# Kernel tuning notes

Measured on AMD Instinct MI355X. Metric: run time of the kernel, lower is better.

## Reference

```python
import jax, jax.numpy as jnp
import numpy as np

STRIDE = 4
ANCHORS = np.array([10.0, 30.0, 60.0], dtype=np.float32)
THRESH = -3.0   # GetPBB confidence threshold
NMS_TH = 0.05   # IoU threshold from nms_idx(pbbs, 0.05)
K_CAND = 4096   # fixed candidate cap for jit-compatible greedy NMS
TOPK = 300      # __get_topk default k


def _decode(output):
    # output: [Z, H, W, A, 5] raw head output -> [N, 5] (score, z, y, x, d)
    Z, H, W, A, _ = output.shape
    dt = output.dtype
    offset = jnp.asarray((STRIDE - 1) / 2.0, dt)
    oz = (offset + STRIDE * jnp.arange(Z, dtype=dt))[:, None, None, None]
    oh = (offset + STRIDE * jnp.arange(H, dtype=dt))[None, :, None, None]
    ow = (offset + STRIDE * jnp.arange(W, dtype=dt))[None, None, :, None]
    anch = jnp.asarray(ANCHORS, dt)[None, None, None, :]
    score = output[..., 0]
    z = oz + output[..., 1] * anch
    y = oh + output[..., 2] * anch
    x = ow + output[..., 3] * anch
    d = jnp.exp(output[..., 4]) * anch
    return jnp.stack([score, z, y, x, d], axis=-1).reshape(-1, 5)


def _iou_matrix(boxes):
    # boxes: [K, 4] = (z, y, x, d) axis-aligned cubes, per iou() in source
    c = boxes[:, :3]
    r = boxes[:, 3:4] * 0.5
    s = c - r  # starts
    e = c + r  # ends
    ov = jnp.maximum(0.0, jnp.minimum(e[:, None, :], e[None, :, :])
                     - jnp.maximum(s[:, None, :], s[None, :, :]))
    inter = ov[..., 0] * ov[..., 1] * ov[..., 2]
    vol = boxes[:, 3] ** 3
    return inter / (vol[:, None] + vol[None, :] - inter)


def reference(output):
    pbb = _decode(output)  # [N, 5]
    # confidence threshold (GetPBB thresh=-3); invalid -> -inf score
    scores = jnp.where(pbb[:, 0] > THRESH, pbb[:, 0], -jnp.inf)
    top_s, idx = jax.lax.top_k(scores, K_CAND)  # sorted descending, as np.argsort(-score)
    cand = pbb[idx]                              # [K_CAND, 5]
    valid = jnp.isfinite(top_s)
    iou = jax.lax.stop_gradient(_iou_matrix(cand[:, 1:5]))  # [K, K]
    ar = jnp.arange(K_CAND)

    def body(i, keep):
        # greedy: box i (if still kept) suppresses all later boxes with IoU >= th
        sup = keep[i] & (iou[i] >= NMS_TH) & (ar > i)
        return keep & ~sup

    keep = jax.lax.fori_loop(0, K_CAND, body, valid)
    final_scores = jnp.where(keep, cand[:, 0], -jnp.inf)
    _, fidx = jax.lax.top_k(final_scores, TOPK)
    return cand[fidx]  # [TOPK, 5] top-k surviving proposals


def setup_inputs() -> dict:
    key = jax.random.key(0)
    output = jax.random.normal(key, (128, 128, 128, 3, 5), dtype=jnp.float32)
    return {"output": output}
```

## Files before the change

kernel.cpp:

```cpp
#include <hip/hip_runtime.h>
#include <stdint.h>

typedef unsigned int u32;
typedef unsigned long long u64;

#define N_BOXES 6291456
#define N_FLOAT4 7864320
#define KCAND 4096
#define TOPK 300
#define CAP 16384
#define SCORE_TH -3.0f
#define NMS_TH 0.05f
#define FIXED_TH 3.0f

#define GLD_LDS16(srcp, dstp) \
    __builtin_amdgcn_global_load_lds( \
        (const __attribute__((address_space(1))) u32*)(srcp), \
        (__attribute__((address_space(3))) u32*)(dstp), 16, 0, 0)

__device__ __forceinline__ u32 sortable(float f) {
    u32 b = __float_as_uint(f);
    return (b & 0x80000000u) ? ~b : (b | 0x80000000u);
}

__device__ __forceinline__ bool quad_score(const float4& v, u32 g, float& s, u32& bidx) {
    u32 r = (4u * g) % 5u;
    if (r == 1u) return false;
    u32 k = (r == 0u) ? 0u : (5u - r);
    s = (k == 0u) ? v.x : ((k == 1u) ? v.y : ((k == 2u) ? v.z : v.w));
    bidx = (4u * g + k) / 5u;
    return true;
}

__global__ __launch_bounds__(256) void k_scan(const float4* __restrict__ in4,
                                              u32* __restrict__ cnt,
                                              u32* __restrict__ ckey, u32* __restrict__ cidx) {
    u32 base = blockIdx.x * 256u + threadIdx.x;
    u32 hits = 0;
#pragma unroll
    for (int k = 0; k < 15; ++k) {
        u32 g = base + (u32)k * 524288u;
        float4 v = in4[g];
        float s; u32 bidx;
        if (quad_score(v, g, s, bidx) && s >= FIXED_TH) hits |= 1u << k;
    }
    while (hits) {
        int k = __builtin_ctz(hits);
        hits &= hits - 1;
        u32 g = base + (u32)k * 524288u;
        float4 v = in4[g];
        float s; u32 bidx;
        if (quad_score(v, g, s, bidx)) {
            u32 pos = atomicAdd(&cnt[0], 1u);
            if (pos < (u32)CAP) { ckey[pos] = sortable(s); cidx[pos] = bidx; }
        }
    }
}

__global__ void k_check(u32* __restrict__ cnt) {
    u32 m = cnt[0];
    u32 ok = (m >= (u32)KCAND && m <= (u32)CAP) ? 1u : 0u;
    cnt[2] = ok;
    if (!ok) cnt[0] = 0;
}

__global__ void k_hist_fb(const float* __restrict__ in, const u32* __restrict__ cnt,
                          u32* __restrict__ hist) {
    if (cnt[2] == 1u) return;
    __shared__ u32 lh[4096];
    for (int k = threadIdx.x; k < 4096; k += blockDim.x) lh[k] = 0;
    __syncthreads();
    int stride = gridDim.x * blockDim.x;
    for (int i = blockIdx.x * blockDim.x + threadIdx.x; i < N_BOXES; i += stride) {
        float f = in[(size_t)i * 5];
        u32 key = (f > SCORE_TH) ? sortable(f) : 0u;
        atomicAdd(&lh[key >> 20], 1u);
    }
    __syncthreads();
    for (int k = threadIdx.x; k < 4096; k += blockDim.x)
        if (lh[k]) atomicAdd(&hist[k], lh[k]);
}

__global__ void k_pivot_fb(const u32* __restrict__ hist, u32* __restrict__ cnt) {
    if (cnt[2] == 1u) return;
    __shared__ u32 part[256];
    int t = threadIdx.x;
    u32 s = 0;
    for (int k = 0; k < 16; ++k) s += hist[t * 16 + k];
    part[t] = s;
    __syncthreads();
    if (t == 0) {
        u32 acc = 0; int chunk = -1;
        for (int c = 255; c >= 0; --c) {
            if (acc + part[c] >= (u32)KCAND) { chunk = c; break; }
            acc += part[c];
        }
        u32 bstar = 0;
        if (chunk >= 0) {
            for (int b = chunk * 16 + 15; b >= chunk * 16; --b) {
                acc += hist[b];
                if (acc >= (u32)KCAND) { bstar = (u32)b; break; }
            }
        }
        cnt[1] = bstar;
    }
}

__global__ void k_compact_fb(const float* __restrict__ in, u32* __restrict__ cnt,
                             u32* __restrict__ ckey, u32* __restrict__ cidx) {
    if (cnt[2] == 1u) return;
    u32 bstar = cnt[1];
    int stride = gridDim.x * blockDim.x;
    for (int i = blockIdx.x * blockDim.x + threadIdx.x; i < N_BOXES; i += stride) {
        float f = in[(size_t)i * 5];
        u32 key = (f > SCORE_TH) ? sortable(f) : 0u;
        if ((key >> 20) >= bstar) {
            u32 pos = atomicAdd(&cnt[0], 1u);
            if (pos < (u32)CAP) { ckey[pos] = key; cidx[pos] = (u32)i; }
        }
    }
}

__global__ void k_rank(const u32* __restrict__ ckey, const u32* __restrict__ cidx,
                       const u32* __restrict__ cnt, u32* __restrict__ rank) {
    int M = (int)min(cnt[0], (u32)CAP);
    int e = blockIdx.x * 256 + threadIdx.x;
    bool act = (e < M);
    u32 mykey = 0, myidx = 0;
    if (act) { mykey = ckey[e]; myidx = cidx[e]; }
    int j0 = blockIdx.y * 1024;
    int j1 = min(j0 + 1024, M);
    __shared__ u32 sk[256], si[256];
    u32 r = 0;
    for (int base = j0; base < j1; base += 256) {
        __syncthreads();
        int jj = base + threadIdx.x;
        if (jj < j1) { sk[threadIdx.x] = ckey[jj]; si[threadIdx.x] = cidx[jj]; }
        __syncthreads();
        int lim = min(256, j1 - base);
        if (act) {
            for (int q = 0; q < lim; ++q) {
                u32 kq = sk[q];
                r += (u32)((kq > mykey) || (kq == mykey && si[q] < myidx));
            }
        }
    }
    if (act && r) atomicAdd(&rank[e], r);
}

__global__ void k_scatter(const u32* __restrict__ ckey, const u32* __restrict__ cidx,
                          const u32* __restrict__ cnt, const u32* __restrict__ rank,
                          u32* __restrict__ skey, u32* __restrict__ sidx) {
    int M = (int)min(cnt[0], (u32)CAP);
    int e = blockIdx.x * 256 + threadIdx.x;
    if (e < M) {
        u32 r = rank[e];
        if (r < (u32)KCAND) { skey[r] = ckey[e]; sidx[r] = cidx[e]; }
    }
}

__global__ void k_decode(const float* __restrict__ in, const u32* __restrict__ skey,
                         const u32* __restrict__ sidx, float* __restrict__ cand,
                         u64* __restrict__ keepg) {
#pragma clang fp contract(off)
    int r = blockIdx.x * 256 + threadIdx.x;
    u32 key = skey[r];
    u32 idx = sidx[r];
    u32 a = idx % 3u;
    u32 rem = idx / 3u;
    u32 w = rem & 127u; rem >>= 7;
    u32 h = rem & 127u;
    u32 z = rem >> 7;
    float anch = (a == 0u) ? 10.0f : ((a == 1u) ? 30.0f : 60.0f);
    const float* p = in + (size_t)idx * 5;
    float s  = p[0];
    float zc = (1.5f + 4.0f * (float)z) + p[1] * anch;
    float yc = (1.5f + 4.0f * (float)h) + p[2] * anch;
    float xc = (1.5f + 4.0f * (float)w) + p[3] * anch;
    float d  = expf(p[4]) * anch;
    float* o = cand + (size_t)r * 5;
    o[0] = s; o[1] = zc; o[2] = yc; o[3] = xc; o[4] = d;
    u64 bal = __ballot(key != 0u);
    if ((threadIdx.x & 63) == 0) keepg[r >> 6] = bal;
}

__global__ void k_mask(const float* __restrict__ cand, u64* __restrict__ mask) {
#pragma clang fp contract(off)
    int i = blockIdx.y;
    int wv = blockIdx.x * 4 + (threadIdx.x >> 6);
    int j = wv * 64 + (threadIdx.x & 63);
    const float* bi = cand + (size_t)i * 5;
    const float* bj = cand + (size_t)j * 5;
    float zi = bi[1], yi = bi[2], xi = bi[3], di = bi[4];
    float zj = bj[1], yj = bj[2], xj = bj[3], dj = bj[4];
    float ri = di * 0.5f, rj = dj * 0.5f;
    float ov0 = fmaxf(0.0f, fminf(zi + ri, zj + rj) - fmaxf(zi - ri, zj - rj));
    float ov1 = fmaxf(0.0f, fminf(yi + ri, yj + rj) - fmaxf(yi - ri, yj - rj));
    float ov2 = fmaxf(0.0f, fminf(xi + ri, xj + rj) - fmaxf(xi - ri, xj - rj));
    float inter = (ov0 * ov1) * ov2;
    float vi = (di * di) * di;
    float vj = (dj * dj) * dj;
    float iou = inter / ((vi + vj) - inter);
    bool bit = (j > i) && (iou >= NMS_TH);
    u64 bal = __ballot(bit);
    if ((threadIdx.x & 63) == 0) mask[(size_t)i * 64 + wv] = bal;
}

__global__ __launch_bounds__(512) void k_nms(const u64* __restrict__ mask,
                                             u64* __restrict__ keepg,
                                             u32* __restrict__ cnt) {
    __shared__ u64 tile[2][4096];
    __shared__ int sstop;
    int lane = threadIdx.x & 63;
    int wave = threadIdx.x >> 6;
    u64 K = (wave == 0) ? keepg[lane] : 0ull;
    int keptTotal = 0;
    if (threadIdx.x == 0) sstop = 64;

    {
        const char* src = (const char*)mask + wave * 4096 + lane * 16;
        char* dst = (char*)&tile[0][0] + wave * 4096;
#pragma unroll
        for (int i = 0; i < 4; ++i)
            GLD_LDS16(src + i * 1024, dst + i * 1024);
    }

    int resolved = 63;
    for (int c = 0; c < 64; ++c) {
        asm volatile("s_waitcnt vmcnt(0)" ::: "memory");
        __syncthreads();
        if (c > sstop) { resolved = sstop; break; }
        const u64* tl = &tile[c & 1][0];
        if (c + 1 < 64) {
            const char* src = (const char*)(mask + (size_t)(c + 1) * 4096) + wave * 4096 + lane * 16;
            char* dst = (char*)&tile[(c + 1) & 1][0] + wave * 4096;
#pragma unroll
            for (int i = 0; i < 4; ++i)
                GLD_LDS16(src + i * 1024, dst + i * 1024);
        }
        if (wave == 0) {
            u64 diag = tl[lane * 64 + c];
            u32 dlo = (u32)diag, dhi = (u32)(diag >> 32);
            u32 kwlo = (u32)__builtin_amdgcn_readlane((int)(u32)K, c);
            u32 kwhi = (u32)__builtin_amdgcn_readlane((int)(u32)(K >> 32), c);
            u64 remaining = ((u64)kwhi << 32) | kwlo;
            u64 kept = 0;
            while (remaining) {
                int b = __builtin_ctzll(remaining);
                kept |= 1ull << b;
                u32 rlo = (u32)__builtin_amdgcn_readlane((int)dlo, b);
                u32 rhi = (u32)__builtin_amdgcn_readlane((int)dhi, b);
                u64 rb = ((u64)rhi << 32) | rlo;
                remaining &= ~(rb | (1ull << b));
            }
            u64 s0 = 0, s1 = 0, s2 = 0, s3 = 0;
#pragma unroll
            for (int b = 0; b < 64; b += 4) {
                u64 m0 = ((kept >> (b + 0)) & 1ull) ? ~0ull : 0ull;
                u64 m1 = ((kept >> (b + 1)) & 1ull) ? ~0ull : 0ull;
                u64 m2 = ((kept >> (b + 2)) & 1ull) ? ~0ull : 0ull;
                u64 m3 = ((kept >> (b + 3)) & 1ull) ? ~0ull : 0ull;
                s0 |= tl[(b + 0) * 64 + lane] & m0;
                s1 |= tl[(b + 1) * 64 + lane] & m1;
                s2 |= tl[(b + 2) * 64 + lane] & m2;
                s3 |= tl[(b + 3) * 64 + lane] & m3;
            }
            K &= ~((s0 | s1) | (s2 | s3));
            keptTotal += (int)__popcll(kept);
            if (lane == 0 && keptTotal >= TOPK && sstop == 64) sstop = c;
        }
    }
    asm volatile("s_waitcnt vmcnt(0)" ::: "memory");
    __syncthreads();
    if (wave == 0) {
        keepg[lane] = K;
        if (lane == 0) cnt[3] = (u32)resolved;
    }
}

__global__ void k_final(const float* __restrict__ cand, const u64* __restrict__ keepg,
                        const u32* __restrict__ cnt, float* __restrict__ outp) {
    __shared__ u64 kw[64];
    __shared__ u32 wp[65];
    int t = threadIdx.x;
    int limit = (int)cnt[3];
    if (t < 64) kw[t] = (t <= limit) ? keepg[t] : 0ull;
    __syncthreads();
    if (t == 0) {
        u32 acc = 0;
        for (int wv = 0; wv < 64; ++wv) { wp[wv] = acc; acc += (u32)__popcll(kw[wv]); }
        wp[64] = acc;
    }
    __syncthreads();
    u32 nk = wp[64];
    int rmax = (limit + 1) * 64;
    for (int r = t; r < rmax; r += 256) {
        u64 word = kw[r >> 6];
        int b = r & 63;
        bool kept = (word >> b) & 1ull;
        u64 lowmask = b ? (~0ull >> (64 - b)) : 0ull;
        u32 before = wp[r >> 6] + (u32)__popcll(word & lowmask);
        u32 slot = kept ? before : (nk + (u32)r - before);
        if (slot < (u32)TOPK) {
            const float* src = cand + (size_t)r * 5;
            float* dst = outp + (size_t)slot * 5;
            dst[0] = src[0]; dst[1] = src[1]; dst[2] = src[2];
            dst[3] = src[3]; dst[4] = src[4];
        }
    }
}

extern "C" void kernel_launch(void* const* d_in, const int* in_sizes, int n_in,
                              void* d_out, int out_size, void* d_ws, size_t ws_size,
                              hipStream_t stream) {
    const float* in = (const float*)d_in[0];
    const float4* in4 = (const float4*)d_in[0];
    float* outp = (float*)d_out;
    char* ws = (char*)d_ws;

    u32* hist = (u32*)(ws + 0);
    u32* cnt  = (u32*)(ws + 16384);
    u32* rank = (u32*)(ws + 16448);
    u32* ckey = (u32*)(ws + 81984);
    u32* cidx = (u32*)(ws + 147520);
    u32* skey = (u32*)(ws + 213056);
    u32* sidx = (u32*)(ws + 229440);
    float* cand = (float*)(ws + 245824);
    u64* keepg  = (u64*)(ws + 327744);
    u64* mask   = (u64*)(ws + 328256);

    hipMemsetAsync(ws, 0, 81984, stream);

    k_scan      <<<2048, 256, 0, stream>>>(in4, cnt, ckey, cidx);
    k_check     <<<1, 1, 0, stream>>>(cnt);
    k_hist_fb   <<<1024, 256, 0, stream>>>(in, cnt, hist);
    k_pivot_fb  <<<1, 256, 0, stream>>>(hist, cnt);
    k_compact_fb<<<1024, 256, 0, stream>>>(in, cnt, ckey, cidx);
    k_rank      <<<dim3(64, 16), 256, 0, stream>>>(ckey, cidx, cnt, rank);
    k_scatter   <<<64, 256, 0, stream>>>(ckey, cidx, cnt, rank, skey, sidx);
    k_decode    <<<16, 256, 0, stream>>>(in, skey, sidx, cand, keepg);
    k_mask      <<<dim3(16, 4096), 256, 0, stream>>>(cand, mask);
    k_nms       <<<1, 512, 0, stream>>>(mask, keepg, cnt);
    k_final     <<<1, 256, 0, stream>>>(cand, keepg, cnt, outp);
}
```

Measured before the change: 175.1 us.

## Load only kept mask rows in NMS via a compact diagonal-block array

k_mask now also writes each row's diagonal 64-bit word into a compact dp array. The NMS kernel shrinks to a single wave and no longer streams the whole 32KB mask tile through LDS with double buffering each chunk. It prefetches the next diagonal block from dp and gathers only the mask rows of kept boxes straight from global memory, eight at a time. This cuts the memory traffic of the serial NMS phase and removes block barriers, but each gather now pays global-load latency where it used to read from LDS.

```diff
diff --git a/kernel.cpp b/kernel.cpp
--- a/kernel.cpp
+++ b/kernel.cpp
@@ -12,11 +12,6 @@
 #define SCORE_TH -3.0f
 #define NMS_TH 0.05f
 #define FIXED_TH 3.0f
-
-#define GLD_LDS16(srcp, dstp) \
-    __builtin_amdgcn_global_load_lds( \
-        (const __attribute__((address_space(1))) u32*)(srcp), \
-        (__attribute__((address_space(3))) u32*)(dstp), 16, 0, 0)
 
 __device__ __forceinline__ u32 sortable(float f) {
     u32 b = __float_as_uint(f);
@@ -184,7 +179,8 @@
     if ((threadIdx.x & 63) == 0) keepg[r >> 6] = bal;
 }
 
-__global__ void k_mask(const float* __restrict__ cand, u64* __restrict__ mask) {
+__global__ void k_mask(const float* __restrict__ cand, u64* __restrict__ mask,
+                       u64* __restrict__ dp) {
 #pragma clang fp contract(off)
     int i = blockIdx.y;
     int wv = blockIdx.x * 4 + (threadIdx.x >> 6);
@@ -203,79 +199,66 @@
     float iou = inter / ((vi + vj) - inter);
     bool bit = (j > i) && (iou >= NMS_TH);
     u64 bal = __ballot(bit);
-    if ((threadIdx.x & 63) == 0) mask[(size_t)i * 64 + wv] = bal;
-}
-
-__global__ __launch_bounds__(512) void k_nms(const u64* __restrict__ mask,
-                                             u64* __restrict__ keepg,
-                                             u32* __restrict__ cnt) {
-    __shared__ u64 tile[2][4096];
-    __shared__ int sstop;
-    int lane = threadIdx.x & 63;
-    int wave = threadIdx.x >> 6;
-    u64 K = (wave == 0) ? keepg[lane] : 0ull;
+    if ((threadIdx.x & 63) == 0) {
+        mask[(size_t)i * 64 + wv] = bal;
+        if (wv == (i >> 6)) dp[i] = bal;
+    }
+}
+
+__global__ __launch_bounds__(64) void k_nms(const u64* __restrict__ mask,
+                                            const u64* __restrict__ dp,
+                                            u64* __restrict__ keepg,
+                                            u32* __restrict__ cnt) {
+    int lane = threadIdx.x;
+    u64 K = keepg[lane];
     int keptTotal = 0;
-    if (threadIdx.x == 0) sstop = 64;
-
-    {
-        const char* src = (const char*)mask + wave * 4096 + lane * 16;
-        char* dst = (char*)&tile[0][0] + wave * 4096;
-#pragma unroll
-        for (int i = 0; i < 4; ++i)
-            GLD_LDS16(src + i * 1024, dst + i * 1024);
-    }
-
     int resolved = 63;
+    u64 dcur = dp[lane];
     for (int c = 0; c < 64; ++c) {
-        asm volatile("s_waitcnt vmcnt(0)" ::: "memory");
-        __syncthreads();
-        if (c > sstop) { resolved = sstop; break; }
-        const u64* tl = &tile[c & 1][0];
-        if (c + 1 < 64) {
-            const char* src = (const char*)(mask + (size_t)(c + 1) * 4096) + wave * 4096 + lane * 16;
-            char* dst = (char*)&tile[(c + 1) & 1][0] + wave * 4096;
-#pragma unroll
-            for (int i = 0; i < 4; ++i)
-                GLD_LDS16(src + i * 1024, dst + i * 1024);
-        }
-        if (wave == 0) {
-            u64 diag = tl[lane * 64 + c];
-            u32 dlo = (u32)diag, dhi = (u32)(diag >> 32);
-            u32 kwlo = (u32)__builtin_amdgcn_readlane((int)(u32)K, c);
-            u32 kwhi = (u32)__builtin_amdgcn_readlane((int)(u32)(K >> 32), c);
-            u64 remaining = ((u64)kwhi << 32) | kwlo;
-            u64 kept = 0;
-            while (remaining) {
-                int b = __builtin_ctzll(remaining);
-                kept |= 1ull << b;
-                u32 rlo = (u32)__builtin_amdgcn_readlane((int)dlo, b);
-                u32 rhi = (u32)__builtin_amdgcn_readlane((int)dhi, b);
-                u64 rb = ((u64)rhi << 32) | rlo;
-                remaining &= ~(rb | (1ull << b));
-            }
-            u64 s0 = 0, s1 = 0, s2 = 0, s3 = 0;
-#pragma unroll
-            for (int b = 0; b < 64; b += 4) {
-                u64 m0 = ((kept >> (b + 0)) & 1ull) ? ~0ull : 0ull;
-                u64 m1 = ((kept >> (b + 1)) & 1ull) ? ~0ull : 0ull;
-                u64 m2 = ((kept >> (b + 2)) & 1ull) ? ~0ull : 0ull;
-                u64 m3 = ((kept >> (b + 3)) & 1ull) ? ~0ull : 0ull;
-                s0 |= tl[(b + 0) * 64 + lane] & m0;
-                s1 |= tl[(b + 1) * 64 + lane] & m1;
-                s2 |= tl[(b + 2) * 64 + lane] & m2;
-                s3 |= tl[(b + 3) * 64 + lane] & m3;
-            }
-            K &= ~((s0 | s1) | (s2 | s3));
-            keptTotal += (int)__popcll(kept);
-            if (lane == 0 && keptTotal >= TOPK && sstop == 64) sstop = c;
-        }
-    }
-    asm volatile("s_waitcnt vmcnt(0)" ::: "memory");
-    __syncthreads();
-    if (wave == 0) {
-        keepg[lane] = K;
-        if (lane == 0) cnt[3] = (u32)resolved;
-    }
+        u64 dnext = (c + 1 < 64) ? dp[(c + 1) * 64 + lane] : 0ull;
+        u32 dlo = (u32)dcur, dhi = (u32)(dcur >> 32);
+        u32 kwlo = (u32)__builtin_amdgcn_readlane((int)(u32)K, c);
+        u32 kwhi = (u32)__builtin_amdgcn_readlane((int)(u32)(K >> 32), c);
+        u64 remaining = ((u64)kwhi << 32) | kwlo;
+        u64 kept = 0;
+        while (remaining) {
+            int b = __builtin_ctzll(remaining);
+            kept |= 1ull << b;
+            u32 rlo = (u32)__builtin_amdgcn_readlane((int)dlo, b);
+            u32 rhi = (u32)__builtin_amdgcn_readlane((int)dhi, b);
+            u64 rb = ((u64)rhi << 32) | rlo;
+            remaining &= ~(rb | (1ull << b));
+        }
+        const u64* rows = mask + (size_t)c * 4096;
+        u64 sup = 0;
+        u64 kk = kept;
+        while (kk) {
+            int b0 = __builtin_ctzll(kk); kk &= kk - 1;
+            int b1 = -1, b2 = -1, b3 = -1, b4 = -1, b5 = -1, b6 = -1, b7 = -1;
+            if (kk) { b1 = __builtin_ctzll(kk); kk &= kk - 1; }
+            if (kk) { b2 = __builtin_ctzll(kk); kk &= kk - 1; }
+            if (kk) { b3 = __builtin_ctzll(kk); kk &= kk - 1; }
+            if (kk) { b4 = __builtin_ctzll(kk); kk &= kk - 1; }
+            if (kk) { b5 = __builtin_ctzll(kk); kk &= kk - 1; }
+            if (kk) { b6 = __builtin_ctzll(kk); kk &= kk - 1; }
+            if (kk) { b7 = __builtin_ctzll(kk); kk &= kk - 1; }
+            u64 v0 = rows[(size_t)b0 * 64 + lane];
+            u64 v1 = (b1 >= 0) ? rows[(size_t)b1 * 64 + lane] : 0ull;
+            u64 v2 = (b2 >= 0) ? rows[(size_t)b2 * 64 + lane] : 0ull;
+            u64 v3 = (b3 >= 0) ? rows[(size_t)b3 * 64 + lane] : 0ull;
+            u64 v4 = (b4 >= 0) ? rows[(size_t)b4 * 64 + lane] : 0ull;
+            u64 v5 = (b5 >= 0) ? rows[(size_t)b5 * 64 + lane] : 0ull;
+            u64 v6 = (b6 >= 0) ? rows[(size_t)b6 * 64 + lane] : 0ull;
+            u64 v7 = (b7 >= 0) ? rows[(size_t)b7 * 64 + lane] : 0ull;
+            sup |= ((v0 | v1) | (v2 | v3)) | ((v4 | v5) | (v6 | v7));
+        }
+        K &= ~sup;
+        keptTotal += (int)__popcll(kept);
+        if (keptTotal >= TOPK) { resolved = c; break; }
+        dcur = dnext;
+    }
+    keepg[lane] = K;
+    if (lane == 0) cnt[3] = (u32)resolved;
 }
 
 __global__ void k_final(const float* __restrict__ cand, const u64* __restrict__ keepg,
@@ -328,6 +311,7 @@
     float* cand = (float*)(ws + 245824);
     u64* keepg  = (u64*)(ws + 327744);
     u64* mask   = (u64*)(ws + 328256);
+    u64* dp     = (u64*)(ws + 2425408);
 
     hipMemsetAsync(ws, 0, 81984, stream);
 
@@ -339,7 +323,7 @@
     k_rank      <<<dim3(64, 16), 256, 0, stream>>>(ckey, cidx, cnt, rank);
     k_scatter   <<<64, 256, 0, stream>>>(ckey, cidx, cnt, rank, skey, sidx);
     k_decode    <<<16, 256, 0, stream>>>(in, skey, sidx, cand, keepg);
-    k_mask      <<<dim3(16, 4096), 256, 0, stream>>>(cand, mask);
-    k_nms       <<<1, 512, 0, stream>>>(mask, keepg, cnt);
+    k_mask      <<<dim3(16, 4096), 256, 0, stream>>>(cand, mask, dp);
+    k_nms       <<<1, 64, 0, stream>>>(mask, dp, keepg, cnt);
     k_final     <<<1, 256, 0, stream>>>(cand, keepg, cnt, outp);
 }
```

Measured after the change: 189.0 us. 1.08x slower.

## Batch 16 rows per mask block and fuse final gather into NMS kernel

Applied to the files above, without the earlier changes.

The IoU mask kernel now processes 16 candidate rows per block, so each thread loads its j box once and reuses it, and the grid shrinks from 65536 to 4096 blocks. The final compaction/gather kernel is folded into the single-block NMS kernel, so the keep bits and resolved count stay in shared memory and one launch plus a global round-trip are removed. This trades some parallelism in the mask kernel for less block-scheduling overhead, and leaves the tail work on a single block.

```diff
diff --git a/kernel.cpp b/kernel.cpp
--- a/kernel.cpp
+++ b/kernel.cpp
@@ -186,31 +186,39 @@
 
 __global__ void k_mask(const float* __restrict__ cand, u64* __restrict__ mask) {
 #pragma clang fp contract(off)
-    int i = blockIdx.y;
     int wv = blockIdx.x * 4 + (threadIdx.x >> 6);
     int j = wv * 64 + (threadIdx.x & 63);
-    const float* bi = cand + (size_t)i * 5;
     const float* bj = cand + (size_t)j * 5;
-    float zi = bi[1], yi = bi[2], xi = bi[3], di = bi[4];
     float zj = bj[1], yj = bj[2], xj = bj[3], dj = bj[4];
-    float ri = di * 0.5f, rj = dj * 0.5f;
-    float ov0 = fmaxf(0.0f, fminf(zi + ri, zj + rj) - fmaxf(zi - ri, zj - rj));
-    float ov1 = fmaxf(0.0f, fminf(yi + ri, yj + rj) - fmaxf(yi - ri, yj - rj));
-    float ov2 = fmaxf(0.0f, fminf(xi + ri, xj + rj) - fmaxf(xi - ri, xj - rj));
-    float inter = (ov0 * ov1) * ov2;
-    float vi = (di * di) * di;
+    float rj = dj * 0.5f;
     float vj = (dj * dj) * dj;
-    float iou = inter / ((vi + vj) - inter);
-    bool bit = (j > i) && (iou >= NMS_TH);
-    u64 bal = __ballot(bit);
-    if ((threadIdx.x & 63) == 0) mask[(size_t)i * 64 + wv] = bal;
+    int i0 = blockIdx.y * 16;
+#pragma unroll
+    for (int ii = 0; ii < 16; ++ii) {
+        int i = i0 + ii;
+        const float* bi = cand + (size_t)i * 5;
+        float zi = bi[1], yi = bi[2], xi = bi[3], di = bi[4];
+        float ri = di * 0.5f;
+        float ov0 = fmaxf(0.0f, fminf(zi + ri, zj + rj) - fmaxf(zi - ri, zj - rj));
+        float ov1 = fmaxf(0.0f, fminf(yi + ri, yj + rj) - fmaxf(yi - ri, yj - rj));
+        float ov2 = fmaxf(0.0f, fminf(xi + ri, xj + rj) - fmaxf(xi - ri, xj - rj));
+        float inter = (ov0 * ov1) * ov2;
+        float vi = (di * di) * di;
+        float iou = inter / ((vi + vj) - inter);
+        bool bit = (j > i) && (iou >= NMS_TH);
+        u64 bal = __ballot(bit);
+        if ((threadIdx.x & 63) == 0) mask[(size_t)i * 64 + wv] = bal;
+    }
 }
 
 __global__ __launch_bounds__(512) void k_nms(const u64* __restrict__ mask,
-                                             u64* __restrict__ keepg,
-                                             u32* __restrict__ cnt) {
+                                             const u64* __restrict__ keepg,
+                                             const float* __restrict__ cand,
+                                             float* __restrict__ outp) {
     __shared__ u64 tile[2][4096];
     __shared__ int sstop;
+    __shared__ u64 kw[64];
+    __shared__ u32 wp[65];
     int lane = threadIdx.x & 63;
     int wave = threadIdx.x >> 6;
     u64 K = (wave == 0) ? keepg[lane] : 0ull;
@@ -272,29 +280,18 @@
     }
     asm volatile("s_waitcnt vmcnt(0)" ::: "memory");
     __syncthreads();
-    if (wave == 0) {
-        keepg[lane] = K;
-        if (lane == 0) cnt[3] = (u32)resolved;
-    }
-}
-
-__global__ void k_final(const float* __restrict__ cand, const u64* __restrict__ keepg,
-                        const u32* __restrict__ cnt, float* __restrict__ outp) {
-    __shared__ u64 kw[64];
-    __shared__ u32 wp[65];
-    int t = threadIdx.x;
-    int limit = (int)cnt[3];
-    if (t < 64) kw[t] = (t <= limit) ? keepg[t] : 0ull;
-    __syncthreads();
-    if (t == 0) {
+
+    if (wave == 0) kw[lane] = (lane <= resolved) ? K : 0ull;
+    __syncthreads();
+    if (threadIdx.x == 0) {
         u32 acc = 0;
-        for (int wv = 0; wv < 64; ++wv) { wp[wv] = acc; acc += (u32)__popcll(kw[wv]); }
+        for (int w2 = 0; w2 < 64; ++w2) { wp[w2] = acc; acc += (u32)__popcll(kw[w2]); }
         wp[64] = acc;
     }
     __syncthreads();
     u32 nk = wp[64];
-    int rmax = (limit + 1) * 64;
-    for (int r = t; r < rmax; r += 256) {
+    int rmax = (resolved + 1) * 64;
+    for (int r = threadIdx.x; r < rmax; r += 512) {
         u64 word = kw[r >> 6];
         int b = r & 63;
         bool kept = (word >> b) & 1ull;
@@ -339,7 +336,6 @@
     k_rank      <<<dim3(64, 16), 256, 0, stream>>>(ckey, cidx, cnt, rank);
     k_scatter   <<<64, 256, 0, stream>>>(ckey, cidx, cnt, rank, skey, sidx);
     k_decode    <<<16, 256, 0, stream>>>(in, skey, sidx, cand, keepg);
-    k_mask      <<<dim3(16, 4096), 256, 0, stream>>>(cand, mask);
-    k_nms       <<<1, 512, 0, stream>>>(mask, keepg, cnt);
-    k_final     <<<1, 256, 0, stream>>>(cand, keepg, cnt, outp);
-}
+    k_mask      <<<dim3(16, 256), 256, 0, stream>>>(cand, mask);
+    k_nms       <<<1, 512, 0, stream>>>(mask, keepg, cand, outp);
+}
```

Measured after the change: 167.7 us. 1.04x faster.
